# Kernel tuning notes

Measured on AMD Instinct MI355X. Metric: run time of the kernel, lower is better.

Reference implementation:

```python
import jax, jax.numpy as jnp
import numpy as np

VOCAB, D = 100000, 128
B, V, L = 2048, 50, 20
N_CLASS = 128

def setup_inputs() -> dict:
    key = jax.random.key(0)
    k1, k2, k3, k4, k5 = jax.random.split(key, 5)
    return {
        "diag_idx": jax.random.randint(k1, (B, V, L), 0, VOCAB),
        "proc_idx": jax.random.randint(k2, (B, V, L), 0, VOCAB),
        "emb": jax.random.normal(k3, (VOCAB, D), dtype=jnp.float32),
        "W": jax.random.normal(k4, (N_CLASS, 2 * D), dtype=jnp.float32) * 0.05,
        "b": jax.random.normal(k5, (N_CLASS,), dtype=jnp.float32) * 0.05,
    }

def _pool(emb, idx):
    # gather [B,V,L,D], mean over codes (dim=1 in torch per-sample == axis 2 here),
    # then sum over visits (dim=0 per-sample == axis 1 here) -> [B, D]
    g = emb[idx]
    return g.mean(axis=2).sum(axis=1)

def reference(diag_idx, proc_idx, emb, W, b):
    d = _pool(emb, diag_idx)            # [B, D]
    p = _pool(emb, proc_idx)            # [B, D]
    x = jnp.concatenate([d, p], axis=-1)  # [B, 2D]
    return x @ W.T + b                  # [B, n_class]
```

## Files before the change

### kernel.cpp

```cpp
#include <hip/hip_runtime.h>


typedef _Float16 h2 __attribute__((ext_vector_type(2)));

constexpr int B      = 2048;
constexpr int V      = 50;
constexpr int L      = 20;
constexpr int D      = 128;
constexpr int NIDX   = V * L;
constexpr int NCLASS = 128;
constexpr int TWO_D  = 2 * D;
constexpr int VOCAB  = 100000;
constexpr int NSLICE = 8;
constexpr int SLICE_ROWS = VOCAB / NSLICE;
constexpr int SROWS_P    = SLICE_ROWS + 1;

__device__ __forceinline__ unsigned short f2bf_rne(float f) {
    unsigned int u = __float_as_uint(f);
    unsigned int r = (u + 0x7FFFu + ((u >> 16) & 1u)) >> 16;
    return (unsigned short)r;
}
__device__ __forceinline__ float uif(unsigned int u) { return __uint_as_float(u); }

__device__ __forceinline__ unsigned int pk_f16(float a, float b) {
    return __builtin_bit_cast(unsigned int, __builtin_amdgcn_cvt_pkrtz(a, b));
}

__global__ __launch_bounds__(256)
void prep_kernel(const float* __restrict__ emb,
                 const int* __restrict__ diag_idx,
                 const int* __restrict__ proc_idx,
                 unsigned short* __restrict__ embb,
                 unsigned short* __restrict__ sorted,
                 int* __restrict__ offs,
                 float* __restrict__ pooled)
{
    const int bid = blockIdx.x;
    const int tid = threadIdx.x;

    if (bid < 12500) {
        const int i4 = bid * 256 + tid;
        const int r  = i4 >> 5;
        const int s  = r / SLICE_ROWS;
        const float4 v = reinterpret_cast<const float4*>(emb)[i4];
        uint2 o;
        o.x = pk_f16(v.x, v.y);
        o.y = pk_f16(v.z, v.w);
        reinterpret_cast<uint2*>(embb)[i4 + s * 32] = o;
        return;
    }
    if (bid == 12500) {
        const int s = tid >> 5, u = tid & 31;
        reinterpret_cast<uint2*>(embb)[((size_t)s * SROWS_P + SLICE_ROWS) * 32 + u] =
            make_uint2(0u, 0u);
        return;
    }

    const int b = bid - 12501;

    __shared__ int cnt[2][NSLICE];
    __shared__ int woff[2][NSLICE];
    __shared__ int offsS[2][NSLICE + 1];
    __shared__ unsigned short sl[2][NIDX];

    if (tid < 16) cnt[tid >> 3][tid & 7] = 0;
    __syncthreads();

    int4 qd = make_int4(0, 0, 0, 0), qp = make_int4(0, 0, 0, 0);
    const bool act = tid < NIDX / 4;
    if (act) {
        qd = reinterpret_cast<const int4*>(diag_idx + (size_t)b * NIDX)[tid];
        qp = reinterpret_cast<const int4*>(proc_idx + (size_t)b * NIDX)[tid];
        atomicAdd(&cnt[0][qd.x / SLICE_ROWS], 1);
        atomicAdd(&cnt[0][qd.y / SLICE_ROWS], 1);
        atomicAdd(&cnt[0][qd.z / SLICE_ROWS], 1);
        atomicAdd(&cnt[0][qd.w / SLICE_ROWS], 1);
        atomicAdd(&cnt[1][qp.x / SLICE_ROWS], 1);
        atomicAdd(&cnt[1][qp.y / SLICE_ROWS], 1);
        atomicAdd(&cnt[1][qp.z / SLICE_ROWS], 1);
        atomicAdd(&cnt[1][qp.w / SLICE_ROWS], 1);
    }
    __syncthreads();

    if (tid < 2) {
        int run = 0;
        for (int k = 0; k < NSLICE; ++k) {
            offsS[tid][k] = run;
            woff[tid][k]  = run;
            run += cnt[tid][k];
        }
        offsS[tid][NSLICE] = run;
    }
    __syncthreads();

    if (act) {
        int s, p;
        s = qd.x / SLICE_ROWS; p = atomicAdd(&woff[0][s], 1); sl[0][p] = (unsigned short)(qd.x - s * SLICE_ROWS);
        s = qd.y / SLICE_ROWS; p = atomicAdd(&woff[0][s], 1); sl[0][p] = (unsigned short)(qd.y - s * SLICE_ROWS);
        s = qd.z / SLICE_ROWS; p = atomicAdd(&woff[0][s], 1); sl[0][p] = (unsigned short)(qd.z - s * SLICE_ROWS);
        s = qd.w / SLICE_ROWS; p = atomicAdd(&woff[0][s], 1); sl[0][p] = (unsigned short)(qd.w - s * SLICE_ROWS);
        s = qp.x / SLICE_ROWS; p = atomicAdd(&woff[1][s], 1); sl[1][p] = (unsigned short)(qp.x - s * SLICE_ROWS);
        s = qp.y / SLICE_ROWS; p = atomicAdd(&woff[1][s], 1); sl[1][p] = (unsigned short)(qp.y - s * SLICE_ROWS);
        s = qp.z / SLICE_ROWS; p = atomicAdd(&woff[1][s], 1); sl[1][p] = (unsigned short)(qp.z - s * SLICE_ROWS);
        s = qp.w / SLICE_ROWS; p = atomicAdd(&woff[1][s], 1); sl[1][p] = (unsigned short)(qp.w - s * SLICE_ROWS);
    }
    __syncthreads();

    unsigned int* so = reinterpret_cast<unsigned int*>(sorted + (size_t)b * 2 * NIDX);
    for (int t = tid; t < NIDX; t += 256) {
        const int h = t / (NIDX / 2), i = t % (NIDX / 2);
        so[t] = (unsigned int)sl[h][2 * i] | ((unsigned int)sl[h][2 * i + 1] << 16);
    }
    if (tid < 2 * (NSLICE + 1))
        offs[b * 2 * (NSLICE + 1) + tid] = offsS[tid / (NSLICE + 1)][tid % (NSLICE + 1)];
    pooled[(size_t)b * TWO_D + tid] = 0.0f;
}

__global__ __launch_bounds__(256, 4)
void slice_pool_kernel(const unsigned short* __restrict__ embb,
                       const unsigned short* __restrict__ sorted,
                       const int* __restrict__ offs,
                       float* __restrict__ pooled)
{
    __shared__ unsigned short lls[2][NIDX + 8];
    __shared__ float part[4][64][9];

    const int slice = blockIdx.x & (NSLICE - 1);
    const int b     = blockIdx.x >> 3;
    const int tid   = threadIdx.x;
    const int lane  = tid & 63;
    const int wave  = tid >> 6;

    const int* ob  = offs + b * 2 * (NSLICE + 1);
    const int beg0 = ob[slice],              n0 = ob[slice + 1] - ob[slice];
    const int beg1 = ob[NSLICE + 1 + slice], n1 = ob[NSLICE + 2 + slice] - ob[NSLICE + 1 + slice];

    const unsigned short* s16 = sorted + (size_t)b * 2 * NIDX;
    for (int i = tid; i < n0; i += 256) lls[0][i] = s16[beg0 + i];
    for (int i = tid; i < n1; i += 256) lls[1][i] = s16[NIDX + beg1 + i];
    if (tid < ((8 - (n0 & 7)) & 7)) lls[0][n0 + tid] = (unsigned short)SLICE_ROWS;
    if (tid < ((8 - (n1 & 7)) & 7)) lls[1][n1 + tid] = (unsigned short)SLICE_ROWS;
    __syncthreads();

    const int h   = wave >> 1;
    const int w2  = wave & 1;
    const int sub = lane >> 4;
    const int c   = lane & 15;
    const int n   = h ? n1 : n0;
    const int n_pad = (n + 7) & ~7;

    const uint4* __restrict__ sbase =
        reinterpret_cast<const uint4*>(embb + (size_t)slice * SROWS_P * D);
    const unsigned short* __restrict__ lb = &lls[h][0];

    h2 acc0 = {0, 0}, acc1 = {0, 0}, acc2 = {0, 0}, acc3 = {0, 0};
    #pragma unroll 4
    for (int i = w2 * 4; i < n_pad; i += 8) {
        const int rl = (int)lb[i + sub];
        const uint4 e = sbase[rl * 16 + c];
        acc0 += __builtin_bit_cast(h2, e.x);
        acc1 += __builtin_bit_cast(h2, e.y);
        acc2 += __builtin_bit_cast(h2, e.z);
        acc3 += __builtin_bit_cast(h2, e.w);
    }
    float* pw = &part[wave][lane][0];
    pw[0] = (float)acc0.x; pw[1] = (float)acc0.y;
    pw[2] = (float)acc1.x; pw[3] = (float)acc1.y;
    pw[4] = (float)acc2.x; pw[5] = (float)acc2.y;
    pw[6] = (float)acc3.x; pw[7] = (float)acc3.y;
    __syncthreads();

    {
        const int hh  = tid >> 7;
        const int dim = tid & 127;
        const int cc  = dim >> 3;
        const int j   = dim & 7;
        float s = 0.f;
        #pragma unroll
        for (int wp = 0; wp < 2; ++wp)
            #pragma unroll
            for (int sb = 0; sb < 4; ++sb)
                s += part[2 * hh + wp][sb * 16 + cc][j];
        atomicAdd(&pooled[(size_t)b * TWO_D + hh * D + dim], s * (1.0f / L));
    }
}

__global__ __launch_bounds__(128)
void head_kernel(const float* __restrict__ pooled,
                 const float* __restrict__ W,
                 const float* __restrict__ bias,
                 float* __restrict__ out)
{
    __shared__ float x[TWO_D];
    const int b   = blockIdx.x;
    const int tid = threadIdx.x;
    x[tid]       = pooled[(size_t)b * TWO_D + tid];
    x[tid + 128] = pooled[(size_t)b * TWO_D + 128 + tid];
    __syncthreads();

    const float4* __restrict__ wrow =
        reinterpret_cast<const float4*>(W + (size_t)tid * TWO_D);
    const float4* __restrict__ xv = reinterpret_cast<const float4*>(x);
    float s = bias[tid];
    #pragma unroll 16
    for (int k = 0; k < TWO_D / 4; ++k) {
        const float4 w4 = wrow[k];
        const float4 x4 = xv[k];
        s = fmaf(w4.x, x4.x, s);
        s = fmaf(w4.y, x4.y, s);
        s = fmaf(w4.z, x4.z, s);
        s = fmaf(w4.w, x4.w, s);
    }
    out[(size_t)b * NCLASS + tid] = s;
}

__global__ __launch_bounds__(256)
void convert_flat_kernel(const float* __restrict__ emb, unsigned short* __restrict__ o)
{
    const int i = blockIdx.x * 256 + threadIdx.x;
    const float4 v = reinterpret_cast<const float4*>(emb)[i];
    ushort4 u;
    u.x = f2bf_rne(v.x); u.y = f2bf_rne(v.y);
    u.z = f2bf_rne(v.z); u.w = f2bf_rne(v.w);
    reinterpret_cast<ushort4*>(o)[i] = u;
}

__global__ __launch_bounds__(256, 4)
void pool_gemm_bf16_kernel(const int* __restrict__ diag_idx,
                           const int* __restrict__ proc_idx,
                           const unsigned short* __restrict__ embb,
                           const float* __restrict__ W,
                           const float* __restrict__ bias,
                           float* __restrict__ out)
{
    __shared__ float4 part4[4][64];
    __shared__ float  x_lds[TWO_D];

    const int b    = blockIdx.x;
    const int tid  = threadIdx.x;
    const int wave = tid >> 6;
    const int lane = tid & 63;

    const int half  = wave >> 1;
    const int chunk = wave & 1;
    const int* __restrict__ idx =
        (half == 0 ? diag_idx : proc_idx) + (size_t)b * NIDX + (size_t)chunk * (NIDX / 2);
    const int2* __restrict__ idx2 = reinterpret_cast<const int2*>(idx);

    const ushort4* __restrict__ emb4 = reinterpret_cast<const ushort4*>(embb);
    const int c = lane & 31;

    float4 acc = make_float4(0.f, 0.f, 0.f, 0.f);
    #pragma unroll 10
    for (int i = 0; i < NIDX / 4; ++i) {
        const int2 p = idx2[i];
        const int  r = (lane & 32) ? p.y : p.x;
        const ushort4 e = emb4[(size_t)r * (D / 4) + c];
        acc.x += uif((unsigned int)e.x << 16);
        acc.y += uif((unsigned int)e.y << 16);
        acc.z += uif((unsigned int)e.z << 16);
        acc.w += uif((unsigned int)e.w << 16);
    }
    part4[wave][lane] = acc;
    __syncthreads();

    {
        const int h   = tid >> 7;
        const int rem = tid & 127;
        const int cc  = rem >> 2;
        const int j   = rem & 3;
        const float* p0 = reinterpret_cast<const float*>(&part4[2 * h][cc]);
        const float* p1 = reinterpret_cast<const float*>(&part4[2 * h][cc + 32]);
        const float* p2 = reinterpret_cast<const float*>(&part4[2 * h + 1][cc]);
        const float* p3 = reinterpret_cast<const float*>(&part4[2 * h + 1][cc + 32]);
        x_lds[tid] = (p0[j] + p1[j] + p2[j] + p3[j]) * (1.0f / L);
    }
    __syncthreads();

    if (tid < NCLASS) {
        const float4* __restrict__ wrow =
            reinterpret_cast<const float4*>(W + (size_t)tid * TWO_D);
        const float4* __restrict__ xv = reinterpret_cast<const float4*>(x_lds);
        float s = bias[tid];
        #pragma unroll 8
        for (int k = 0; k < TWO_D / 4; ++k) {
            const float4 w4 = wrow[k];
            const float4 x4 = xv[k];
            s = fmaf(w4.x, x4.x, s);
            s = fmaf(w4.y, x4.y, s);
            s = fmaf(w4.z, x4.z, s);
            s = fmaf(w4.w, x4.w, s);
        }
        out[(size_t)b * NCLASS + tid] = s;
    }
}

__global__ __launch_bounds__(256, 4)
void pool_gemm_f32_kernel(const int* __restrict__ diag_idx,
                          const int* __restrict__ proc_idx,
                          const float* __restrict__ emb,
                          const float* __restrict__ W,
                          const float* __restrict__ bias,
                          float* __restrict__ out)
{
    __shared__ float4 part4[4][64];
    __shared__ float  x_lds[TWO_D];

    const int b    = blockIdx.x;
    const int tid  = threadIdx.x;
    const int wave = tid >> 6;
    const int lane = tid & 63;

    const int half  = wave >> 1;
    const int chunk = wave & 1;
    const int* __restrict__ idx =
        (half == 0 ? diag_idx : proc_idx) + (size_t)b * NIDX + (size_t)chunk * (NIDX / 2);
    const int2* __restrict__ idx2 = reinterpret_cast<const int2*>(idx);

    const float4* __restrict__ emb4 = reinterpret_cast<const float4*>(emb);
    const int c = lane & 31;

    float4 acc = make_float4(0.f, 0.f, 0.f, 0.f);
    #pragma unroll 5
    for (int i = 0; i < NIDX / 4; ++i) {
        const int2 p = idx2[i];
        const int  r = (lane & 32) ? p.y : p.x;
        const float4 e = emb4[(size_t)r * (D / 4) + c];
        acc.x += e.x; acc.y += e.y; acc.z += e.z; acc.w += e.w;
    }
    part4[wave][lane] = acc;
    __syncthreads();

    {
        const int h   = tid >> 7;
        const int rem = tid & 127;
        const int cc  = rem >> 2;
        const int j   = rem & 3;
        const float* p0 = reinterpret_cast<const float*>(&part4[2 * h][cc]);
        const float* p1 = reinterpret_cast<const float*>(&part4[2 * h][cc + 32]);
        const float* p2 = reinterpret_cast<const float*>(&part4[2 * h + 1][cc]);
        const float* p3 = reinterpret_cast<const float*>(&part4[2 * h + 1][cc + 32]);
        x_lds[tid] = (p0[j] + p1[j] + p2[j] + p3[j]) * (1.0f / L);
    }
    __syncthreads();

    if (tid < NCLASS) {
        const float4* __restrict__ wrow =
            reinterpret_cast<const float4*>(W + (size_t)tid * TWO_D);
        const float4* __restrict__ xv = reinterpret_cast<const float4*>(x_lds);
        float s = bias[tid];
        #pragma unroll 8
        for (int k = 0; k < TWO_D / 4; ++k) {
            const float4 w4 = wrow[k];
            const float4 x4 = xv[k];
            s = fmaf(w4.x, x4.x, s);
            s = fmaf(w4.y, x4.y, s);
            s = fmaf(w4.z, x4.z, s);
            s = fmaf(w4.w, x4.w, s);
        }
        out[(size_t)b * NCLASS + tid] = s;
    }
}

extern "C" void kernel_launch(void* const* d_in, const int* in_sizes, int n_in,
                              void* d_out, int out_size, void* d_ws, size_t ws_size,
                              hipStream_t stream)
{
    const int*   diag = (const int*)d_in[0];
    const int*   proc = (const int*)d_in[1];
    const float* emb  = (const float*)d_in[2];
    const float* W    = (const float*)d_in[3];
    const float* bias = (const float*)d_in[4];
    float*       out  = (float*)d_out;

    const size_t embb_bytes   = (size_t)NSLICE * SROWS_P * D * sizeof(unsigned short);
    const size_t sorted_bytes = (size_t)B * 2 * NIDX * sizeof(unsigned short);
    const size_t offs_bytes   = (size_t)B * 2 * (NSLICE + 1) * sizeof(int);
    const size_t pooled_bytes = (size_t)B * TWO_D * sizeof(float);
    const size_t need = embb_bytes + sorted_bytes + offs_bytes + pooled_bytes;

    const size_t emb_flat_bytes = (size_t)VOCAB * D * sizeof(unsigned short);

    if (ws_size >= need) {
        char* p = (char*)d_ws;
        unsigned short* embb   = (unsigned short*)p;              p += embb_bytes;
        unsigned short* sorted = (unsigned short*)p;              p += sorted_bytes;
        int*            offs   = (int*)p;                         p += offs_bytes;
        float*          pooled = (float*)p;

        prep_kernel<<<12501 + B, 256, 0, stream>>>(emb, diag, proc,
                                                   embb, sorted, offs, pooled);
        slice_pool_kernel<<<B * NSLICE, 256, 0, stream>>>(embb, sorted, offs, pooled);
        head_kernel<<<B, 128, 0, stream>>>(pooled, W, bias, out);
    } else if (ws_size >= emb_flat_bytes) {
        unsigned short* embb = (unsigned short*)d_ws;
        convert_flat_kernel<<<(VOCAB * D / 4) / 256, 256, 0, stream>>>(emb, embb);
        pool_gemm_bf16_kernel<<<B, 256, 0, stream>>>(diag, proc, embb, W, bias, out);
    } else {
        pool_gemm_f32_kernel<<<B, 256, 0, stream>>>(diag, proc, emb, W, bias, out);
    }
}
```

Measured before the change: 180.5 us.

## Replace atomic slice reduction with per-wave partials reduced in head kernel

The slice pooling kernel now gives each wave one (sample, half, slice) list, read straight from global memory instead of being staged in LDS. Each block covers two samples, and partial sums are reduced within the wave by shuffles. The per-slice fp16 partials are written to a buffer, and the head kernel sums them over slices before the GEMV. This removes the float atomics, the pooled zeroing, the LDS staging and the block barriers, and raises the occupancy hint. In exchange it adds an extra partial buffer and keeps fp16 accumulation per slice, which carries some overflow and precision risk.

Result: slower. 185.4 us (+2.7%).

```diff
diff --git a/kernel.cpp b/kernel.cpp
--- a/kernel.cpp
+++ b/kernel.cpp
@@ -25,6 +25,9 @@
 __device__ __forceinline__ unsigned int pk_f16(float a, float b) {
     return __builtin_bit_cast(unsigned int, __builtin_amdgcn_cvt_pkrtz(a, b));
 }
+__device__ __forceinline__ h2 h2_shfl_xor(h2 a, int m) {
+    return __builtin_bit_cast(h2, __shfl_xor(__builtin_bit_cast(int, a), m, 64));
+}
 
 __global__ __launch_bounds__(256)
 void prep_kernel(const float* __restrict__ emb,
@@ -32,8 +35,7 @@
                  const int* __restrict__ proc_idx,
                  unsigned short* __restrict__ embb,
                  unsigned short* __restrict__ sorted,
-                 int* __restrict__ offs,
-                 float* __restrict__ pooled)
+                 int* __restrict__ offs)
 {
     const int bid = blockIdx.x;
     const int tid = threadIdx.x;
@@ -113,80 +115,65 @@
     }
     if (tid < 2 * (NSLICE + 1))
         offs[b * 2 * (NSLICE + 1) + tid] = offsS[tid / (NSLICE + 1)][tid % (NSLICE + 1)];
-    pooled[(size_t)b * TWO_D + tid] = 0.0f;
-}
-
-__global__ __launch_bounds__(256, 4)
+}
+
+__global__ __launch_bounds__(256, 6)
 void slice_pool_kernel(const unsigned short* __restrict__ embb,
                        const unsigned short* __restrict__ sorted,
                        const int* __restrict__ offs,
-                       float* __restrict__ pooled)
-{
-    __shared__ unsigned short lls[2][NIDX + 8];
-    __shared__ float part[4][64][9];
-
-    const int slice = blockIdx.x & (NSLICE - 1);
-    const int b     = blockIdx.x >> 3;
-    const int tid   = threadIdx.x;
-    const int lane  = tid & 63;
-    const int wave  = tid >> 6;
-
-    const int* ob  = offs + b * 2 * (NSLICE + 1);
-    const int beg0 = ob[slice],              n0 = ob[slice + 1] - ob[slice];
-    const int beg1 = ob[NSLICE + 1 + slice], n1 = ob[NSLICE + 2 + slice] - ob[NSLICE + 1 + slice];
-
-    const unsigned short* s16 = sorted + (size_t)b * 2 * NIDX;
-    for (int i = tid; i < n0; i += 256) lls[0][i] = s16[beg0 + i];
-    for (int i = tid; i < n1; i += 256) lls[1][i] = s16[NIDX + beg1 + i];
-    if (tid < ((8 - (n0 & 7)) & 7)) lls[0][n0 + tid] = (unsigned short)SLICE_ROWS;
-    if (tid < ((8 - (n1 & 7)) & 7)) lls[1][n1 + tid] = (unsigned short)SLICE_ROWS;
-    __syncthreads();
-
-    const int h   = wave >> 1;
-    const int w2  = wave & 1;
+                       unsigned int* __restrict__ pooledp)
+{
+    const int bid  = blockIdx.x;
+    const int s    = bid & (NSLICE - 1);
+    const int bq   = bid >> 3;
+    const int tid  = threadIdx.x;
+    const int wave = tid >> 6;
+    const int lane = tid & 63;
+    const int b    = bq * 2 + (wave >> 1);
+    const int h    = wave & 1;
+
+    const int* ob  = offs + (b * 2 + h) * (NSLICE + 1);
+    const int beg  = ob[s];
+    const int n    = ob[s + 1] - beg;
+
+    const unsigned short* __restrict__ lst =
+        sorted + (size_t)(b * 2 + h) * NIDX + beg;
+    const uint4* __restrict__ sbase =
+        reinterpret_cast<const uint4*>(embb + (size_t)s * SROWS_P * D);
+
     const int sub = lane >> 4;
     const int c   = lane & 15;
-    const int n   = h ? n1 : n0;
-    const int n_pad = (n + 7) & ~7;
-
-    const uint4* __restrict__ sbase =
-        reinterpret_cast<const uint4*>(embb + (size_t)slice * SROWS_P * D);
-    const unsigned short* __restrict__ lb = &lls[h][0];
-
-    h2 acc0 = {0, 0}, acc1 = {0, 0}, acc2 = {0, 0}, acc3 = {0, 0};
-    #pragma unroll 4
-    for (int i = w2 * 4; i < n_pad; i += 8) {
-        const int rl = (int)lb[i + sub];
+
+    h2 a0 = {0, 0}, a1 = {0, 0}, a2 = {0, 0}, a3 = {0, 0};
+    #pragma unroll 8
+    for (int i = 0; i < n; i += 4) {
+        const int j  = i + sub;
+        const int rv = (int)lst[j];
+        const int rl = (j < n) ? rv : SLICE_ROWS;
         const uint4 e = sbase[rl * 16 + c];
-        acc0 += __builtin_bit_cast(h2, e.x);
-        acc1 += __builtin_bit_cast(h2, e.y);
-        acc2 += __builtin_bit_cast(h2, e.z);
-        acc3 += __builtin_bit_cast(h2, e.w);
-    }
-    float* pw = &part[wave][lane][0];
-    pw[0] = (float)acc0.x; pw[1] = (float)acc0.y;
-    pw[2] = (float)acc1.x; pw[3] = (float)acc1.y;
-    pw[4] = (float)acc2.x; pw[5] = (float)acc2.y;
-    pw[6] = (float)acc3.x; pw[7] = (float)acc3.y;
-    __syncthreads();
-
-    {
-        const int hh  = tid >> 7;
-        const int dim = tid & 127;
-        const int cc  = dim >> 3;
-        const int j   = dim & 7;
-        float s = 0.f;
-        #pragma unroll
-        for (int wp = 0; wp < 2; ++wp)
-            #pragma unroll
-            for (int sb = 0; sb < 4; ++sb)
-                s += part[2 * hh + wp][sb * 16 + cc][j];
-        atomicAdd(&pooled[(size_t)b * TWO_D + hh * D + dim], s * (1.0f / L));
+        a0 += __builtin_bit_cast(h2, e.x);
+        a1 += __builtin_bit_cast(h2, e.y);
+        a2 += __builtin_bit_cast(h2, e.z);
+        a3 += __builtin_bit_cast(h2, e.w);
+    }
+
+    a0 += h2_shfl_xor(a0, 16); a1 += h2_shfl_xor(a1, 16);
+    a2 += h2_shfl_xor(a2, 16); a3 += h2_shfl_xor(a3, 16);
+    a0 += h2_shfl_xor(a0, 32); a1 += h2_shfl_xor(a1, 32);
+    a2 += h2_shfl_xor(a2, 32); a3 += h2_shfl_xor(a3, 32);
+
+    if (lane < 16) {
+        uint4 o;
+        o.x = __builtin_bit_cast(unsigned int, a0);
+        o.y = __builtin_bit_cast(unsigned int, a1);
+        o.z = __builtin_bit_cast(unsigned int, a2);
+        o.w = __builtin_bit_cast(unsigned int, a3);
+        reinterpret_cast<uint4*>(pooledp + ((size_t)((b * 2 + h) * NSLICE + s) * 64))[c] = o;
     }
 }
 
 __global__ __launch_bounds__(128)
-void head_kernel(const float* __restrict__ pooled,
+void head_kernel(const unsigned int* __restrict__ pooledp,
                  const float* __restrict__ W,
                  const float* __restrict__ bias,
                  float* __restrict__ out)
@@ -194,24 +181,35 @@
     __shared__ float x[TWO_D];
     const int b   = blockIdx.x;
     const int tid = threadIdx.x;
-    x[tid]       = pooled[(size_t)b * TWO_D + tid];
-    x[tid + 128] = pooled[(size_t)b * TWO_D + 128 + tid];
+    const int h   = tid >> 6;
+    const int c2  = tid & 63;
+
+    const unsigned int* pp = pooledp + (size_t)(b * 2 + h) * NSLICE * 64 + c2;
+    float sx = 0.f, sy = 0.f;
+    #pragma unroll
+    for (int sl = 0; sl < NSLICE; ++sl) {
+        const h2 v = __builtin_bit_cast(h2, pp[sl * 64]);
+        sx += (float)v.x;
+        sy += (float)v.y;
+    }
+    x[h * D + 2 * c2]     = sx * (1.0f / L);
+    x[h * D + 2 * c2 + 1] = sy * (1.0f / L);
     __syncthreads();
 
     const float4* __restrict__ wrow =
         reinterpret_cast<const float4*>(W + (size_t)tid * TWO_D);
     const float4* __restrict__ xv = reinterpret_cast<const float4*>(x);
-    float s = bias[tid];
+    float acc = bias[tid];
     #pragma unroll 16
     for (int k = 0; k < TWO_D / 4; ++k) {
         const float4 w4 = wrow[k];
         const float4 x4 = xv[k];
-        s = fmaf(w4.x, x4.x, s);
-        s = fmaf(w4.y, x4.y, s);
-        s = fmaf(w4.z, x4.z, s);
-        s = fmaf(w4.w, x4.w, s);
-    }
-    out[(size_t)b * NCLASS + tid] = s;
+        acc = fmaf(w4.x, x4.x, acc);
+        acc = fmaf(w4.y, x4.y, acc);
+        acc = fmaf(w4.z, x4.z, acc);
+        acc = fmaf(w4.w, x4.w, acc);
+    }
+    out[(size_t)b * NCLASS + tid] = acc;
 }
 
 __global__ __launch_bounds__(256)
@@ -373,25 +371,24 @@
     const float* bias = (const float*)d_in[4];
     float*       out  = (float*)d_out;
 
-    const size_t embb_bytes   = (size_t)NSLICE * SROWS_P * D * sizeof(unsigned short);
-    const size_t sorted_bytes = (size_t)B * 2 * NIDX * sizeof(unsigned short);
-    const size_t offs_bytes   = (size_t)B * 2 * (NSLICE + 1) * sizeof(int);
-    const size_t pooled_bytes = (size_t)B * TWO_D * sizeof(float);
-    const size_t need = embb_bytes + sorted_bytes + offs_bytes + pooled_bytes;
+    const size_t embb_bytes    = (size_t)NSLICE * SROWS_P * D * sizeof(unsigned short);
+    const size_t sorted_bytes  = (size_t)B * 2 * NIDX * sizeof(unsigned short) + 16;
+    const size_t offs_bytes    = (size_t)B * 2 * (NSLICE + 1) * sizeof(int);
+    const size_t pooledp_bytes = (size_t)B * 2 * NSLICE * 64 * sizeof(unsigned int);
+    const size_t need = embb_bytes + sorted_bytes + offs_bytes + pooledp_bytes;
 
     const size_t emb_flat_bytes = (size_t)VOCAB * D * sizeof(unsigned short);
 
     if (ws_size >= need) {
         char* p = (char*)d_ws;
-        unsigned short* embb   = (unsigned short*)p;              p += embb_bytes;
-        unsigned short* sorted = (unsigned short*)p;              p += sorted_bytes;
-        int*            offs   = (int*)p;                         p += offs_bytes;
-        float*          pooled = (float*)p;
-
-        prep_kernel<<<12501 + B, 256, 0, stream>>>(emb, diag, proc,
-                                                   embb, sorted, offs, pooled);
-        slice_pool_kernel<<<B * NSLICE, 256, 0, stream>>>(embb, sorted, offs, pooled);
-        head_kernel<<<B, 128, 0, stream>>>(pooled, W, bias, out);
+        unsigned short* embb    = (unsigned short*)p;             p += embb_bytes;
+        unsigned short* sorted  = (unsigned short*)p;             p += sorted_bytes;
+        int*            offs    = (int*)p;                        p += offs_bytes;
+        unsigned int*   pooledp = (unsigned int*)p;
+
+        prep_kernel<<<12501 + B, 256, 0, stream>>>(emb, diag, proc, embb, sorted, offs);
+        slice_pool_kernel<<<(B / 2) * NSLICE, 256, 0, stream>>>(embb, sorted, offs, pooledp);
+        head_kernel<<<B, 128, 0, stream>>>(pooledp, W, bias, out);
     } else if (ws_size >= emb_flat_bytes) {
         unsigned short* embb = (unsigned short*)d_ws;
         convert_flat_kernel<<<(VOCAB * D / 4) / 256, 256, 0, stream>>>(emb, embb);
```
